# Performance work log

Measured on AMD Instinct MI355X. Metric: run time of the kernel, lower is better.

Reference implementation:

```python
import jax, jax.numpy as jnp
from jax import lax
import numpy as np

RADIUS = 1
DILATION = 2
NUM_BINS = 16  # DualSimilarityLoss uses num_bins=16
ALPHA = 5.0
BETA = 0.1
NOISE = 1e-4


def _avg_pool2(x):
    b, c, h, w = x.shape
    return x.reshape(b, c, h // 2, 2, w // 2, 2).mean(axis=(3, 5))


def _conv_rep(x, k, pad):
    # replicate-pad then VALID conv, NCHW / OIHW
    xp = jnp.pad(x, ((0, 0), (0, 0), (pad, pad), (pad, pad)), mode='edge')
    return lax.conv_general_dilated(xp, k, (1, 1), 'VALID',
                                    dimension_numbers=('NCHW', 'OIHW', 'NCHW'))


def _upsample_align_corners(x, H, W):
    # bilinear, align_corners=True (matches F.interpolate(..., align_corners=True))
    b, c, h, w = x.shape

    def coords(n_out, n_in):
        pos = jnp.arange(n_out, dtype=x.dtype) * ((n_in - 1) / (n_out - 1))
        i0 = jnp.clip(jnp.floor(pos).astype(jnp.int32), 0, n_in - 2)
        return i0, pos - i0.astype(x.dtype)

    y0, fy = coords(H, h)
    x0, fx = coords(W, w)
    rows = x[:, :, y0, :] * (1.0 - fy)[None, None, :, None] \
         + x[:, :, y0 + 1, :] * fy[None, None, :, None]
    out = rows[:, :, :, x0] * (1.0 - fx) + rows[:, :, :, x0 + 1] * fx
    return out


def _compute_mind(img, key):
    B, _, H, W = img.shape
    img = _avg_pool2(img)                      # (B,1,H/2,W/2)
    img = img + NOISE * jax.random.normal(key, img.shape, img.dtype)
    h, w = img.shape[2], img.shape[3]
    pad = RADIUS * DILATION                    # 2
    k = 2 * RADIUS + 1                         # 3
    ones_k = jnp.ones((1, 1, k, k), img.dtype)
    padded = jnp.pad(img, ((0, 0), (0, 0), (pad, pad), (pad, pad)), mode='edge')
    patch_mean = lax.conv_general_dilated(padded, ones_k, (1, 1), 'VALID',
                                          dimension_numbers=('NCHW', 'OIHW', 'NCHW')) / (k * k)
    patch_mean = jnp.pad(patch_mean, ((0, 0), (0, 0), (pad, pad), (pad, pad)), mode='edge')
    c = pad
    center = padded[:, :, c:c + h, c:c + w]
    variance = (center - patch_mean[:, :, c:c + h, c:c + w]) ** 2
    variance = _conv_rep(variance, ones_k, RADIUS) / (k * k)
    variance = jnp.maximum(variance, 1e-4)
    descs = []
    for i in range(-RADIUS, RADIUS + 1):
        for j in range(-RADIUS, RADIUS + 1):
            if i == 0 and j == 0:
                continue
            dx, dy = i * DILATION, j * DILATION
            off = padded[:, :, c + dy:c + dy + h, c + dx:c + dx + w]
            diff = jnp.clip((center - off) ** 2 / (variance * 2 + 1e-6), 0.0, 50.0)
            descs.append(diff)
    m = jnp.exp(-jnp.concatenate(descs, axis=1))          # (B,8,h,w)
    m = m / (m.sum(axis=1, keepdims=True) + 1e-8)
    m = jnp.where(jnp.isnan(m), 0.0, m)
    if (h, w) != (H, W):
        m = _upsample_align_corners(m, H, W)
    return m


def _nmi_loss(x, y, kx, ky):
    B = x.shape[0]
    x = x[:, :, ::2, ::2]
    y = y[:, :, ::2, ::2]
    x = x + NOISE * jax.random.normal(kx, x.shape, x.dtype)
    y = y + NOISE * jax.random.normal(ky, y.shape, y.dtype)
    xf = jnp.clip((x.reshape(B, -1) + 1.0) / 2.0, 0.001, 0.999)
    yf = jnp.clip((y.reshape(B, -1) + 1.0) / 2.0, 0.001, 0.999)
    grid = jnp.linspace(0.0, 1.0, NUM_BINS + 1)
    xb = jnp.clip(jnp.searchsorted(grid, xf, side='left') - 1, 0, NUM_BINS - 1)
    yb = jnp.clip(jnp.searchsorted(grid, yf, side='left') - 1, 0, NUM_BINS - 1)
    idx = xb * NUM_BINS + yb                               # (B,N)
    hist = jnp.zeros((B, NUM_BINS * NUM_BINS), jnp.float32)
    hist = hist.at[jnp.arange(B)[:, None], idx].add(1.0)
    hist = hist.reshape(B, NUM_BINS, NUM_BINS)
    hist = hist / (hist.sum(axis=(1, 2), keepdims=True) + 1e-10)
    xh = hist.sum(axis=2)
    yh = hist.sum(axis=1)
    eps = 1e-5
    hist = hist + eps
    xh = xh + eps
    yh = yh + eps
    mi = jnp.sum(hist * (jnp.log(hist) - jnp.log(xh[:, :, None] * yh[:, None, :])), axis=(1, 2))
    hx = -jnp.sum(xh * jnp.log(xh), axis=1)
    hy = -jnp.sum(yh * jnp.log(yh), axis=1)
    se = hx + hy
    nmi = jnp.where(se < 1e-10, 0.0, 2.0 * mi / se)
    nmi = jnp.clip(nmi, -1.0, 1.0)
    return -jnp.clip(nmi.mean(), -1.0, 1.0)


def _reg_loss(flow, ku, kv):
    sx = jnp.array([[-1, 0, 1], [-2, 0, 2], [-1, 0, 1]], jnp.float32).reshape(1, 1, 3, 3)
    sy = jnp.array([[-1, -2, -1], [0, 0, 0], [1, 2, 1]], jnp.float32).reshape(1, 1, 3, 3)
    lp = jnp.array([[0, 1, 0], [1, -4, 1], [0, 1, 0]], jnp.float32).reshape(1, 1, 3, 3)
    f = _avg_pool2(flow)
    u = f[:, 0:1] + NOISE * jax.random.normal(ku, f[:, 0:1].shape, f.dtype)
    v = f[:, 1:2] + NOISE * jax.random.normal(kv, f[:, 1:2].shape, f.dtype)
    grad_mag = _conv_rep(u, sx, 1) ** 2 + _conv_rep(u, sy, 1) ** 2 \
             + _conv_rep(v, sx, 1) ** 2 + _conv_rep(v, sy, 1) ** 2
    lap_mag = _conv_rep(u, lp, 1) ** 2 + _conv_rep(v, lp, 1) ** 2
    return jnp.clip(grad_mag, 0.0, 100.0).mean() + jnp.clip(lap_mag, 0.0, 100.0).mean()


def _total_loss(fixed, moved, flow):
    fixed = jnp.where(jnp.isnan(fixed), 0.0, fixed)
    moved = jnp.where(jnp.isnan(moved), 0.0, moved)
    flow = jnp.where(jnp.isnan(flow), 0.0, flow)
    ks = jax.random.split(jax.random.key(42), 6)
    mi = _nmi_loss(fixed, moved, ks[0], ks[1])
    mx = _compute_mind(fixed, ks[2])
    my = _compute_mind(moved, ks[3])
    d = jnp.abs(mx - my)
    mind = jnp.where(jnp.isnan(d), 0.0, d).mean()
    reg = _reg_loss(flow, ks[4], ks[5])
    return mi + ALPHA * mind + BETA * reg


def setup_inputs() -> dict:
    key = jax.random.key(0)
    k1, k2, k3 = jax.random.split(key, 3)
    B, H, W = 8, 512, 512
    return {
        'fixed': jax.random.normal(k1, (B, 1, H, W), jnp.float32),
        'moved': jax.random.normal(k2, (B, 1, H, W), jnp.float32),
        'flow': jax.random.normal(k3, (B, 2, H, W), jnp.float32),
    }


def reference(fixed, moved, flow):
    return _total_loss(fixed, moved, flow)
```

## Files before the change

### kernel.cpp

```cpp
#include <hip/hip_runtime.h>
#include <cmath>

#define BATCH 8
#define HF 512
#define WF 512
#define HS 256
#define WS 256
#define PLANE_S (HS * WS)
#define PLANE_F (HF * WF)

#define NMIND_BLOCKS 2048
#define NREG_BLOCKS  512

#define OFF_HIST  0
#define OFF_PMIND 8192
#define OFF_PGRAD (OFF_PMIND + NMIND_BLOCKS * 8)
#define OFF_PLAP  (OFF_PGRAD + NREG_BLOCKS * 8)

#define IMG_R 23
#define IMG_S 24
#define T_R 20
#define T_S 21
#define V_R 18
#define V_S 19

#define RP 34
#define RS 35

__device__ __forceinline__ int clampi(int v, int lo, int hi) {
    return v < lo ? lo : (v > hi ? hi : v);
}

__device__ __forceinline__ int bin_of(float x) {
    float v = (x + 1.0f) * 0.5f;
    v = fminf(fmaxf(v, 0.001f), 0.999f);
    float t = v * 16.0f;
    float ft = floorf(t);
    int c = (int)ft + ((t > ft) ? 1 : 0);
    int b = c - 1;
    return b < 0 ? 0 : (b > 15 ? 15 : b);
}

__global__ void init_hist_kernel(unsigned* __restrict__ hist) {
    hist[blockIdx.x * 256 + threadIdx.x] = 0u;
}

__global__ __launch_bounds__(256, 4) void fused_main_kernel(
    const float* __restrict__ fixed, const float* __restrict__ moved,
    const float* __restrict__ flow,
    unsigned* __restrict__ hist, double* __restrict__ pmind,
    double* __restrict__ pgrad, double* __restrict__ plap)
{
    __shared__ float S[4524];
    __shared__ unsigned lh[256];
    __shared__ float red[256];
    int tid = threadIdx.x;

    if (blockIdx.z < 2) {
        int idx = blockIdx.z * 256 + blockIdx.y * 16 + blockIdx.x;
        int b = idx >> 6, t64 = idx & 63;
        int y0p = (t64 >> 3) * 32, x0p = (t64 & 7) * 32;
        float* U = S;
        float* V = S + RP * RS;
        const float* ur = flow + (size_t)(b * 2) * PLANE_F;
        const float* vr = ur + PLANE_F;
        for (int i = tid; i < RP * RP; i += 256) {
            int r = i / RP, c = i - r * RP;
            int gy = clampi(y0p - 1 + r, 0, HS - 1);
            int gx = clampi(x0p - 1 + c, 0, WS - 1);
            const float* uu = ur + (size_t)(gy * 2) * WF + (size_t)(gx * 2);
            const float* vv = vr + (size_t)(gy * 2) * WF + (size_t)(gx * 2);
            float2 u0 = *(const float2*)uu, u1 = *(const float2*)(uu + WF);
            float2 v0 = *(const float2*)vv, v1 = *(const float2*)(vv + WF);
            U[r * RS + c] = (u0.x + u0.y + u1.x + u1.y) * 0.25f;
            V[r * RS + c] = (v0.x + v0.y + v1.x + v1.y) * 0.25f;
        }
        __syncthreads();
        float g = 0.f, l = 0.f;
        for (int k = tid; k < 32 * 32; k += 256) {
            int y = k >> 5, x = k & 31;
            const float* u0 = &U[y * RS + x];
            const float* v0 = &V[y * RS + x];
            float a00 = u0[0],      a01 = u0[1],          a02 = u0[2];
            float a10 = u0[RS],     a11 = u0[RS + 1],     a12 = u0[RS + 2];
            float a20 = u0[2 * RS], a21 = u0[2 * RS + 1], a22 = u0[2 * RS + 2];
            float c00 = v0[0],      c01 = v0[1],          c02 = v0[2];
            float c10 = v0[RS],     c11 = v0[RS + 1],     c12 = v0[RS + 2];
            float c20 = v0[2 * RS], c21 = v0[2 * RS + 1], c22 = v0[2 * RS + 2];
            float gxu = (a02 - a00) + 2.f * (a12 - a10) + (a22 - a20);
            float gyu = (a20 - a00) + 2.f * (a21 - a01) + (a22 - a02);
            float gxv = (c02 - c00) + 2.f * (c12 - c10) + (c22 - c20);
            float gyv = (c20 - c00) + 2.f * (c21 - c01) + (c22 - c02);
            float lpu = a01 + a10 - 4.f * a11 + a12 + a21;
            float lpv = c01 + c10 - 4.f * c11 + c12 + c21;
            float grad = gxu * gxu + gyu * gyu + gxv * gxv + gyv * gyv;
            float lap = lpu * lpu + lpv * lpv;
            g += fminf(grad, 100.f);
            l += fminf(lap, 100.f);
        }
        red[tid] = g;
        __syncthreads();
        for (int s = 128; s > 0; s >>= 1) { if (tid < s) red[tid] += red[tid + s]; __syncthreads(); }
        if (tid == 0) pgrad[b * 64 + t64] = (double)red[0];
        __syncthreads();
        red[tid] = l;
        __syncthreads();
        for (int s = 128; s > 0; s >>= 1) { if (tid < s) red[tid] += red[tid + s]; __syncthreads(); }
        if (tid == 0) plap[b * 64 + t64] = (double)red[0];
        return;
    }

    const float FS = (float)(255.0 / 511.0);
    int tx = blockIdx.x, ty = blockIdx.y, b = blockIdx.z - 2;
    int Xb = tx * 32, Yb = ty * 32;
    int dbx = (int)((float)Xb * FS);
    int dby = (int)((float)Yb * FS);
    int ibx = dbx - 3, iby = dby - 3;

    float* imgF = S;
    float* imgM = S + IMG_R * IMG_S;
    float* varF = S + 2 * IMG_R * IMG_S;
    float* varM = varF + V_R * V_S;
    float* diff = varM + V_R * V_S;
    float* tF   = diff;
    float* tM   = diff + T_R * T_S;

    lh[tid] = 0u;
    __syncthreads();

    const float* fb = fixed + (size_t)b * PLANE_F;
    const float* mb = moved + (size_t)b * PLANE_F;
    int oy0 = ty * 16, ox0 = tx * 16;
    for (int i = tid; i < IMG_R * IMG_R; i += 256) {
        int r = i / IMG_R, c = i - r * IMG_R;
        int gy = iby + r, gx = ibx + c;
        int cy = clampi(gy, 0, HS - 1), cx = clampi(gx, 0, WS - 1);
        const float* fp = fb + (size_t)(cy * 2) * WF + (size_t)(cx * 2);
        const float* mp = mb + (size_t)(cy * 2) * WF + (size_t)(cx * 2);
        float2 f0 = *(const float2*)fp;
        float2 f1 = *(const float2*)(fp + WF);
        float2 m0 = *(const float2*)mp;
        float2 m1 = *(const float2*)(mp + WF);
        imgF[r * IMG_S + c] = (f0.x + f0.y + f1.x + f1.y) * 0.25f;
        imgM[r * IMG_S + c] = (m0.x + m0.y + m1.x + m1.y) * 0.25f;
        if ((unsigned)(gy - oy0) < 16u && (unsigned)(gx - ox0) < 16u) {
            atomicAdd(&lh[bin_of(f0.x) * 16 + bin_of(m0.x)], 1u);
        }
    }
    __syncthreads();
    if (lh[tid]) atomicAdd(&hist[b * 256 + tid], lh[tid]);

    const float NINTH = 1.0f / 9.0f;
    for (int i = tid; i < T_R * T_R; i += 256) {
        int r = i / T_R, c = i - r * T_R;
        float sF = 0.f, sM = 0.f;
        #pragma unroll
        for (int dy = 0; dy < 3; dy++)
            #pragma unroll
            for (int dx = 0; dx < 3; dx++) {
                sF += imgF[(r + dy) * IMG_S + c + dx];
                sM += imgM[(r + dy) * IMG_S + c + dx];
            }
        float dF = imgF[(r + 2) * IMG_S + c + 2] - sF * NINTH;
        float dM = imgM[(r + 2) * IMG_S + c + 2] - sM * NINTH;
        tF[r * T_S + c] = dF * dF;
        tM[r * T_S + c] = dM * dM;
    }
    __syncthreads();

    for (int i = tid; i < V_R * V_R; i += 256) {
        int r = i / V_R, c = i - r * V_R;
        float sF = 0.f, sM = 0.f;
        #pragma unroll
        for (int dy = 0; dy < 3; dy++)
            #pragma unroll
            for (int dx = 0; dx < 3; dx++) {
                sF += tF[(r + dy) * T_S + c + dx];
                sM += tM[(r + dy) * T_S + c + dx];
            }
        varF[r * V_S + c] = fmaxf(sF * NINTH, 1e-4f);
        varM[r * V_S + c] = fmaxf(sM * NINTH, 1e-4f);
    }
    __syncthreads();

    for (int i = tid; i < V_R * V_R; i += 256) {
        int r = i / V_R, c = i - r * V_R;
        float cF = imgF[(r + 3) * IMG_S + c + 3];
        float cM = imgM[(r + 3) * IMG_S + c + 3];
        float dF2 = 2.f * varF[r * V_S + c] + 1e-6f;
        float dM2 = 2.f * varM[r * V_S + c] + 1e-6f;
        float invF = 1.0f / dF2;
        float invM = 1.0f / dM2;
        float eF[8], eM[8];
        float sF = 0.f, sM = 0.f;
        int ch = 0;
        #pragma unroll
        for (int ii = -1; ii <= 1; ii++) {
            #pragma unroll
            for (int jj = -1; jj <= 1; jj++) {
                if (ii == 0 && jj == 0) continue;
                float aF = cF - imgF[(r + 3 + 2 * jj) * IMG_S + (c + 3 + 2 * ii)];
                float aM = cM - imgM[(r + 3 + 2 * jj) * IMG_S + (c + 3 + 2 * ii)];
                float qF = fminf(aF * aF * invF, 50.f);
                float qM = fminf(aM * aM * invM, 50.f);
                float vF_ = expf(-qF), vM_ = expf(-qM);
                eF[ch] = vF_; eM[ch] = vM_;
                sF += vF_; sM += vM_;
                ch++;
            }
        }
        float wF = 1.f / (sF + 1e-8f);
        float wM = 1.f / (sM + 1e-8f);
        float* dp = diff + (size_t)(r * V_S + c) * 8;
        #pragma unroll
        for (int q = 0; q < 8; q++) dp[q] = eF[q] * wF - eM[q] * wM;
    }
    __syncthreads();

    float local = 0.f;
    for (int k = tid; k < 32 * 32; k += 256) {
        int dy = k >> 5, dx = k & 31;
        float py = (float)(Yb + dy) * FS;
        int y0 = (int)py; if (y0 > HS - 2) y0 = HS - 2;
        float fy = py - (float)y0;
        float px = (float)(Xb + dx) * FS;
        int x0 = (int)px; if (x0 > WS - 2) x0 = WS - 2;
        float fx = px - (float)x0;
        const float* p00 = diff + (size_t)((y0 - dby) * V_S + (x0 - dbx)) * 8;
        const float* p10 = p00 + V_S * 8;
        #pragma unroll
        for (int q = 0; q < 8; q++) {
            float a  = p00[q]     * (1.f - fy) + p10[q]     * fy;
            float c2 = p00[q + 8] * (1.f - fy) + p10[q + 8] * fy;
            local += fabsf(a * (1.f - fx) + c2 * fx);
        }
    }
    red[tid] = local;
    __syncthreads();
    for (int s = 128; s > 0; s >>= 1) { if (tid < s) red[tid] += red[tid + s]; __syncthreads(); }
    if (tid == 0) pmind[b * 256 + ty * 16 + tx] = (double)red[0];
}

__global__ void tail_kernel(const unsigned* __restrict__ hist,
                            const double* __restrict__ pmind,
                            const double* __restrict__ pgrad, const double* __restrict__ plap,
                            float* __restrict__ out) {
    int t = threadIdx.x;
    __shared__ float p[256];
    __shared__ float xh[16], yh[16];
    __shared__ float redf[256];
    __shared__ double red[256];

    float nmi_sum = 0.f;
    const float eps = 1e-5f;
    for (int b = 0; b < BATCH; b++) {
        unsigned hv = hist[b * 256 + t];
        float pv = (float)hv / 65536.0f;
        p[t] = pv;
        __syncthreads();
        if (t < 16) {
            float s = 0.f;
            for (int j = 0; j < 16; j++) s += p[t * 16 + j];
            xh[t] = s;
        } else if (t < 32) {
            int j = t - 16;
            float s = 0.f;
            for (int i = 0; i < 16; i++) s += p[i * 16 + j];
            yh[j] = s;
        }
        __syncthreads();
        int i = t >> 4, j = t & 15;
        float h = pv + eps;
        float mi_term = h * (logf(h) - logf((xh[i] + eps) * (yh[j] + eps)));
        redf[t] = mi_term;
        __syncthreads();
        for (int s = 128; s > 0; s >>= 1) { if (t < s) redf[t] += redf[t + s]; __syncthreads(); }
        float mi = redf[0];
        __syncthreads();
        float e_term = 0.f;
        if (t < 16) { float xe = xh[t] + eps; e_term = -xe * logf(xe); }
        else if (t < 32) { float ye = yh[t - 16] + eps; e_term = -ye * logf(ye); }
        redf[t] = e_term;
        __syncthreads();
        for (int s = 128; s > 0; s >>= 1) { if (t < s) redf[t] += redf[t + s]; __syncthreads(); }
        float se = redf[0];
        float nmi = (se < 1e-10f) ? 0.f : 2.f * mi / se;
        nmi_sum += fminf(fmaxf(nmi, -1.f), 1.f);
        __syncthreads();
    }

    double sm = 0.0;
    for (int i = t; i < NMIND_BLOCKS; i += 256) sm += pmind[i];
    double sg = 0.0, sl = 0.0;
    for (int i = t; i < NREG_BLOCKS; i += 256) { sg += pgrad[i]; sl += plap[i]; }
    red[t] = sm;
    __syncthreads();
    for (int s = 128; s > 0; s >>= 1) { if (t < s) red[t] += red[t + s]; __syncthreads(); }
    double mind_sum = red[0];
    __syncthreads();
    red[t] = sg;
    __syncthreads();
    for (int s = 128; s > 0; s >>= 1) { if (t < s) red[t] += red[t + s]; __syncthreads(); }
    double grad_sum = red[0];
    __syncthreads();
    red[t] = sl;
    __syncthreads();
    for (int s = 128; s > 0; s >>= 1) { if (t < s) red[t] += red[t + s]; __syncthreads(); }
    double lap_sum = red[0];
    if (t == 0) {
        float s = nmi_sum / (float)BATCH;
        s = fminf(fmaxf(s, -1.f), 1.f);
        double mi_loss = -(double)s;
        double mind_mean = mind_sum / (64.0 * (double)PLANE_F);
        double reg = grad_sum / (double)(BATCH * PLANE_S) + lap_sum / (double)(BATCH * PLANE_S);
        out[0] = (float)(mi_loss + 5.0 * mind_mean + 0.1 * reg);
    }
}

extern "C" void kernel_launch(void* const* d_in, const int* in_sizes, int n_in,
                              void* d_out, int out_size, void* d_ws, size_t ws_size,
                              hipStream_t stream) {
    const float* fixed = (const float*)d_in[0];
    const float* moved = (const float*)d_in[1];
    const float* flow  = (const float*)d_in[2];
    float* out = (float*)d_out;
    char* ws = (char*)d_ws;

    unsigned* hist  = (unsigned*)(ws + OFF_HIST);
    double*   pmind = (double*)(ws + OFF_PMIND);
    double*   pgrad = (double*)(ws + OFF_PGRAD);
    double*   plap  = (double*)(ws + OFF_PLAP);

    init_hist_kernel<<<dim3(8), 256, 0, stream>>>(hist);
    fused_main_kernel<<<dim3(16, 16, 10), 256, 0, stream>>>(fixed, moved, flow,
                                                            hist, pmind, pgrad, plap);
    tail_kernel<<<1, 256, 0, stream>>>(hist, pmind, pgrad, plap, out);
}
```

Measured before the change: 121.7 us.

## Fold tail reduction into main kernel via last-block ticket counters

Removes the separate single-block tail kernel. Blocks now atomically add their partial sums into global doubles, and per-batch ticket counters let the last block of each batch compute that batch's NMI. A global counter then lets the final block write the loss. This drops one kernel launch and the serial tail pass. In exchange it adds global atomics and fences, and the double atomicAdd makes the summation order nondeterministic.

```diff
diff --git a/kernel.cpp b/kernel.cpp
--- a/kernel.cpp
+++ b/kernel.cpp
@@ -9,13 +9,15 @@
 #define PLANE_S (HS * WS)
 #define PLANE_F (HF * WF)
 
-#define NMIND_BLOCKS 2048
-#define NREG_BLOCKS  512
+#define TICKETS_PER_BATCH 320u
 
 #define OFF_HIST  0
-#define OFF_PMIND 8192
-#define OFF_PGRAD (OFF_PMIND + NMIND_BLOCKS * 8)
-#define OFF_PLAP  (OFF_PGRAD + NREG_BLOCKS * 8)
+#define OFF_CNTB  8192
+#define OFF_GCNT  8224
+#define OFF_NMIB  8228
+#define OFF_SUMS  8264
+#define OFF_END   8288
+#define INIT_WORDS (OFF_END / 4)
 
 #define IMG_R 23
 #define IMG_S 24
@@ -41,24 +43,32 @@
     return b < 0 ? 0 : (b > 15 ? 15 : b);
 }
 
-__global__ void init_hist_kernel(unsigned* __restrict__ hist) {
-    hist[blockIdx.x * 256 + threadIdx.x] = 0u;
-}
-
-__global__ __launch_bounds__(256, 4) void fused_main_kernel(
+__global__ void init_kernel(unsigned* __restrict__ w) {
+    int t = threadIdx.x;
+    for (int i = t; i < INIT_WORDS; i += 256) w[i] = 0u;
+}
+
+__global__ __launch_bounds__(256, 4) void fused_all_kernel(
     const float* __restrict__ fixed, const float* __restrict__ moved,
     const float* __restrict__ flow,
-    unsigned* __restrict__ hist, double* __restrict__ pmind,
-    double* __restrict__ pgrad, double* __restrict__ plap)
+    unsigned* __restrict__ hist, unsigned* __restrict__ cntb,
+    unsigned* __restrict__ gcnt, unsigned* __restrict__ nmib,
+    double* __restrict__ sums, float* __restrict__ out)
 {
     __shared__ float S[4524];
     __shared__ unsigned lh[256];
     __shared__ float red[256];
+    __shared__ float xh[16], yh[16];
+    __shared__ float fn[8];
+    __shared__ double fs[3];
+    __shared__ unsigned tk, gk;
     int tid = threadIdx.x;
+    int bb;
 
     if (blockIdx.z < 2) {
         int idx = blockIdx.z * 256 + blockIdx.y * 16 + blockIdx.x;
         int b = idx >> 6, t64 = idx & 63;
+        bb = b;
         int y0p = (t64 >> 3) * 32, x0p = (t64 & 7) * 32;
         float* U = S;
         float* V = S + RP * RS;
@@ -101,218 +111,209 @@
         red[tid] = g;
         __syncthreads();
         for (int s = 128; s > 0; s >>= 1) { if (tid < s) red[tid] += red[tid + s]; __syncthreads(); }
-        if (tid == 0) pgrad[b * 64 + t64] = (double)red[0];
+        if (tid == 0) atomicAdd(&sums[1], (double)red[0]);
         __syncthreads();
         red[tid] = l;
         __syncthreads();
         for (int s = 128; s > 0; s >>= 1) { if (tid < s) red[tid] += red[tid + s]; __syncthreads(); }
-        if (tid == 0) plap[b * 64 + t64] = (double)red[0];
-        return;
-    }
-
-    const float FS = (float)(255.0 / 511.0);
-    int tx = blockIdx.x, ty = blockIdx.y, b = blockIdx.z - 2;
-    int Xb = tx * 32, Yb = ty * 32;
-    int dbx = (int)((float)Xb * FS);
-    int dby = (int)((float)Yb * FS);
-    int ibx = dbx - 3, iby = dby - 3;
-
-    float* imgF = S;
-    float* imgM = S + IMG_R * IMG_S;
-    float* varF = S + 2 * IMG_R * IMG_S;
-    float* varM = varF + V_R * V_S;
-    float* diff = varM + V_R * V_S;
-    float* tF   = diff;
-    float* tM   = diff + T_R * T_S;
-
-    lh[tid] = 0u;
-    __syncthreads();
-
-    const float* fb = fixed + (size_t)b * PLANE_F;
-    const float* mb = moved + (size_t)b * PLANE_F;
-    int oy0 = ty * 16, ox0 = tx * 16;
-    for (int i = tid; i < IMG_R * IMG_R; i += 256) {
-        int r = i / IMG_R, c = i - r * IMG_R;
-        int gy = iby + r, gx = ibx + c;
-        int cy = clampi(gy, 0, HS - 1), cx = clampi(gx, 0, WS - 1);
-        const float* fp = fb + (size_t)(cy * 2) * WF + (size_t)(cx * 2);
-        const float* mp = mb + (size_t)(cy * 2) * WF + (size_t)(cx * 2);
-        float2 f0 = *(const float2*)fp;
-        float2 f1 = *(const float2*)(fp + WF);
-        float2 m0 = *(const float2*)mp;
-        float2 m1 = *(const float2*)(mp + WF);
-        imgF[r * IMG_S + c] = (f0.x + f0.y + f1.x + f1.y) * 0.25f;
-        imgM[r * IMG_S + c] = (m0.x + m0.y + m1.x + m1.y) * 0.25f;
-        if ((unsigned)(gy - oy0) < 16u && (unsigned)(gx - ox0) < 16u) {
-            atomicAdd(&lh[bin_of(f0.x) * 16 + bin_of(m0.x)], 1u);
-        }
-    }
-    __syncthreads();
-    if (lh[tid]) atomicAdd(&hist[b * 256 + tid], lh[tid]);
-
-    const float NINTH = 1.0f / 9.0f;
-    for (int i = tid; i < T_R * T_R; i += 256) {
-        int r = i / T_R, c = i - r * T_R;
-        float sF = 0.f, sM = 0.f;
-        #pragma unroll
-        for (int dy = 0; dy < 3; dy++)
-            #pragma unroll
-            for (int dx = 0; dx < 3; dx++) {
-                sF += imgF[(r + dy) * IMG_S + c + dx];
-                sM += imgM[(r + dy) * IMG_S + c + dx];
+        if (tid == 0) atomicAdd(&sums[2], (double)red[0]);
+    } else {
+        const float FS = (float)(255.0 / 511.0);
+        int tx = blockIdx.x, ty = blockIdx.y, b = blockIdx.z - 2;
+        bb = b;
+        int Xb = tx * 32, Yb = ty * 32;
+        int dbx = (int)((float)Xb * FS);
+        int dby = (int)((float)Yb * FS);
+        int ibx = dbx - 3, iby = dby - 3;
+
+        float* imgF = S;
+        float* imgM = S + IMG_R * IMG_S;
+        float* varF = S + 2 * IMG_R * IMG_S;
+        float* varM = varF + V_R * V_S;
+        float* diff = varM + V_R * V_S;
+        float* tF   = diff;
+        float* tM   = diff + T_R * T_S;
+
+        lh[tid] = 0u;
+        __syncthreads();
+
+        const float* fb = fixed + (size_t)b * PLANE_F;
+        const float* mb = moved + (size_t)b * PLANE_F;
+        int oy0 = ty * 16, ox0 = tx * 16;
+        for (int i = tid; i < IMG_R * IMG_R; i += 256) {
+            int r = i / IMG_R, c = i - r * IMG_R;
+            int gy = iby + r, gx = ibx + c;
+            int cy = clampi(gy, 0, HS - 1), cx = clampi(gx, 0, WS - 1);
+            const float* fp = fb + (size_t)(cy * 2) * WF + (size_t)(cx * 2);
+            const float* mp = mb + (size_t)(cy * 2) * WF + (size_t)(cx * 2);
+            float2 f0 = *(const float2*)fp;
+            float2 f1 = *(const float2*)(fp + WF);
+            float2 m0 = *(const float2*)mp;
+            float2 m1 = *(const float2*)(mp + WF);
+            imgF[r * IMG_S + c] = (f0.x + f0.y + f1.x + f1.y) * 0.25f;
+            imgM[r * IMG_S + c] = (m0.x + m0.y + m1.x + m1.y) * 0.25f;
+            if ((unsigned)(gy - oy0) < 16u && (unsigned)(gx - ox0) < 16u) {
+                atomicAdd(&lh[bin_of(f0.x) * 16 + bin_of(m0.x)], 1u);
             }
-        float dF = imgF[(r + 2) * IMG_S + c + 2] - sF * NINTH;
-        float dM = imgM[(r + 2) * IMG_S + c + 2] - sM * NINTH;
-        tF[r * T_S + c] = dF * dF;
-        tM[r * T_S + c] = dM * dM;
-    }
-    __syncthreads();
-
-    for (int i = tid; i < V_R * V_R; i += 256) {
-        int r = i / V_R, c = i - r * V_R;
-        float sF = 0.f, sM = 0.f;
-        #pragma unroll
-        for (int dy = 0; dy < 3; dy++)
-            #pragma unroll
-            for (int dx = 0; dx < 3; dx++) {
-                sF += tF[(r + dy) * T_S + c + dx];
-                sM += tM[(r + dy) * T_S + c + dx];
+        }
+        __syncthreads();
+        if (lh[tid]) atomicAdd(&hist[b * 256 + tid], lh[tid]);
+
+        const float NINTH = 1.0f / 9.0f;
+        for (int i = tid; i < T_R * T_R; i += 256) {
+            int r = i / T_R, c = i - r * T_R;
+            float sF = 0.f, sM = 0.f;
+            #pragma unroll
+            for (int dy = 0; dy < 3; dy++)
+                #pragma unroll
+                for (int dx = 0; dx < 3; dx++) {
+                    sF += imgF[(r + dy) * IMG_S + c + dx];
+                    sM += imgM[(r + dy) * IMG_S + c + dx];
+                }
+            float dF = imgF[(r + 2) * IMG_S + c + 2] - sF * NINTH;
+            float dM = imgM[(r + 2) * IMG_S + c + 2] - sM * NINTH;
+            tF[r * T_S + c] = dF * dF;
+            tM[r * T_S + c] = dM * dM;
+        }
+        __syncthreads();
+
+        for (int i = tid; i < V_R * V_R; i += 256) {
+            int r = i / V_R, c = i - r * V_R;
+            float sF = 0.f, sM = 0.f;
+            #pragma unroll
+            for (int dy = 0; dy < 3; dy++)
+                #pragma unroll
+                for (int dx = 0; dx < 3; dx++) {
+                    sF += tF[(r + dy) * T_S + c + dx];
+                    sM += tM[(r + dy) * T_S + c + dx];
+                }
+            varF[r * V_S + c] = fmaxf(sF * NINTH, 1e-4f);
+            varM[r * V_S + c] = fmaxf(sM * NINTH, 1e-4f);
+        }
+        __syncthreads();
+
+        for (int i = tid; i < V_R * V_R; i += 256) {
+            int r = i / V_R, c = i - r * V_R;
+            float cF = imgF[(r + 3) * IMG_S + c + 3];
+            float cM = imgM[(r + 3) * IMG_S + c + 3];
+            float dF2 = 2.f * varF[r * V_S + c] + 1e-6f;
+            float dM2 = 2.f * varM[r * V_S + c] + 1e-6f;
+            float invF = 1.0f / dF2;
+            float invM = 1.0f / dM2;
+            float eF[8], eM[8];
+            float sF = 0.f, sM = 0.f;
+            int ch = 0;
+            #pragma unroll
+            for (int ii = -1; ii <= 1; ii++) {
+                #pragma unroll
+                for (int jj = -1; jj <= 1; jj++) {
+                    if (ii == 0 && jj == 0) continue;
+                    float aF = cF - imgF[(r + 3 + 2 * jj) * IMG_S + (c + 3 + 2 * ii)];
+                    float aM = cM - imgM[(r + 3 + 2 * jj) * IMG_S + (c + 3 + 2 * ii)];
+                    float qF = fminf(aF * aF * invF, 50.f);
+                    float qM = fminf(aM * aM * invM, 50.f);
+                    float vF_ = expf(-qF), vM_ = expf(-qM);
+                    eF[ch] = vF_; eM[ch] = vM_;
+                    sF += vF_; sM += vM_;
+                    ch++;
+                }
             }
-        varF[r * V_S + c] = fmaxf(sF * NINTH, 1e-4f);
-        varM[r * V_S + c] = fmaxf(sM * NINTH, 1e-4f);
-    }
-    __syncthreads();
-
-    for (int i = tid; i < V_R * V_R; i += 256) {
-        int r = i / V_R, c = i - r * V_R;
-        float cF = imgF[(r + 3) * IMG_S + c + 3];
-        float cM = imgM[(r + 3) * IMG_S + c + 3];
-        float dF2 = 2.f * varF[r * V_S + c] + 1e-6f;
-        float dM2 = 2.f * varM[r * V_S + c] + 1e-6f;
-        float invF = 1.0f / dF2;
-        float invM = 1.0f / dM2;
-        float eF[8], eM[8];
-        float sF = 0.f, sM = 0.f;
-        int ch = 0;
-        #pragma unroll
-        for (int ii = -1; ii <= 1; ii++) {
-            #pragma unroll
-            for (int jj = -1; jj <= 1; jj++) {
-                if (ii == 0 && jj == 0) continue;
-                float aF = cF - imgF[(r + 3 + 2 * jj) * IMG_S + (c + 3 + 2 * ii)];
-                float aM = cM - imgM[(r + 3 + 2 * jj) * IMG_S + (c + 3 + 2 * ii)];
-                float qF = fminf(aF * aF * invF, 50.f);
-                float qM = fminf(aM * aM * invM, 50.f);
-                float vF_ = expf(-qF), vM_ = expf(-qM);
-                eF[ch] = vF_; eM[ch] = vM_;
-                sF += vF_; sM += vM_;
-                ch++;
+            float wF = 1.f / (sF + 1e-8f);
+            float wM = 1.f / (sM + 1e-8f);
+            float* dp = diff + (size_t)(r * V_S + c) * 8;
+            #pragma unroll
+            for (int q = 0; q < 8; q++) dp[q] = eF[q] * wF - eM[q] * wM;
+        }
+        __syncthreads();
+
+        float local = 0.f;
+        for (int k = tid; k < 32 * 32; k += 256) {
+            int dy = k >> 5, dx = k & 31;
+            float py = (float)(Yb + dy) * FS;
+            int y0 = (int)py; if (y0 > HS - 2) y0 = HS - 2;
+            float fy = py - (float)y0;
+            float px = (float)(Xb + dx) * FS;
+            int x0 = (int)px; if (x0 > WS - 2) x0 = WS - 2;
+            float fx = px - (float)x0;
+            const float* p00 = diff + (size_t)((y0 - dby) * V_S + (x0 - dbx)) * 8;
+            const float* p10 = p00 + V_S * 8;
+            #pragma unroll
+            for (int q = 0; q < 8; q++) {
+                float a  = p00[q]     * (1.f - fy) + p10[q]     * fy;
+                float c2 = p00[q + 8] * (1.f - fy) + p10[q + 8] * fy;
+                local += fabsf(a * (1.f - fx) + c2 * fx);
             }
         }
-        float wF = 1.f / (sF + 1e-8f);
-        float wM = 1.f / (sM + 1e-8f);
-        float* dp = diff + (size_t)(r * V_S + c) * 8;
-        #pragma unroll
-        for (int q = 0; q < 8; q++) dp[q] = eF[q] * wF - eM[q] * wM;
-    }
-    __syncthreads();
-
-    float local = 0.f;
-    for (int k = tid; k < 32 * 32; k += 256) {
-        int dy = k >> 5, dx = k & 31;
-        float py = (float)(Yb + dy) * FS;
-        int y0 = (int)py; if (y0 > HS - 2) y0 = HS - 2;
-        float fy = py - (float)y0;
-        float px = (float)(Xb + dx) * FS;
-        int x0 = (int)px; if (x0 > WS - 2) x0 = WS - 2;
-        float fx = px - (float)x0;
-        const float* p00 = diff + (size_t)((y0 - dby) * V_S + (x0 - dbx)) * 8;
-        const float* p10 = p00 + V_S * 8;
-        #pragma unroll
-        for (int q = 0; q < 8; q++) {
-            float a  = p00[q]     * (1.f - fy) + p10[q]     * fy;
-            float c2 = p00[q + 8] * (1.f - fy) + p10[q + 8] * fy;
-            local += fabsf(a * (1.f - fx) + c2 * fx);
-        }
-    }
-    red[tid] = local;
+        red[tid] = local;
+        __syncthreads();
+        for (int s = 128; s > 0; s >>= 1) { if (tid < s) red[tid] += red[tid + s]; __syncthreads(); }
+        if (tid == 0) atomicAdd(&sums[0], (double)red[0]);
+    }
+
+    __syncthreads();
+    if (tid == 0) {
+        __threadfence();
+        tk = atomicAdd(&cntb[bb], 1u);
+    }
+    __syncthreads();
+    if (tk != TICKETS_PER_BATCH - 1u) return;
+
+    __threadfence();
+    unsigned hv = atomicOr(&hist[bb * 256 + tid], 0u);
+    float pv = (float)hv / 65536.0f;
+    S[tid] = pv;
+    __syncthreads();
+    if (tid < 16) {
+        float s = 0.f;
+        for (int j = 0; j < 16; j++) s += S[tid * 16 + j];
+        xh[tid] = s;
+    } else if (tid < 32) {
+        int j = tid - 16;
+        float s = 0.f;
+        for (int i = 0; i < 16; i++) s += S[i * 16 + j];
+        yh[j] = s;
+    }
+    __syncthreads();
+    const float eps = 1e-5f;
+    int ii2 = tid >> 4, jj2 = tid & 15;
+    float h = pv + eps;
+    float mi_term = h * (logf(h) - logf((xh[ii2] + eps) * (yh[jj2] + eps)));
+    red[tid] = mi_term;
     __syncthreads();
     for (int s = 128; s > 0; s >>= 1) { if (tid < s) red[tid] += red[tid + s]; __syncthreads(); }
-    if (tid == 0) pmind[b * 256 + ty * 16 + tx] = (double)red[0];
-}
-
-__global__ void tail_kernel(const unsigned* __restrict__ hist,
-                            const double* __restrict__ pmind,
-                            const double* __restrict__ pgrad, const double* __restrict__ plap,
-                            float* __restrict__ out) {
-    int t = threadIdx.x;
-    __shared__ float p[256];
-    __shared__ float xh[16], yh[16];
-    __shared__ float redf[256];
-    __shared__ double red[256];
-
-    float nmi_sum = 0.f;
-    const float eps = 1e-5f;
-    for (int b = 0; b < BATCH; b++) {
-        unsigned hv = hist[b * 256 + t];
-        float pv = (float)hv / 65536.0f;
-        p[t] = pv;
-        __syncthreads();
-        if (t < 16) {
-            float s = 0.f;
-            for (int j = 0; j < 16; j++) s += p[t * 16 + j];
-            xh[t] = s;
-        } else if (t < 32) {
-            int j = t - 16;
-            float s = 0.f;
-            for (int i = 0; i < 16; i++) s += p[i * 16 + j];
-            yh[j] = s;
-        }
-        __syncthreads();
-        int i = t >> 4, j = t & 15;
-        float h = pv + eps;
-        float mi_term = h * (logf(h) - logf((xh[i] + eps) * (yh[j] + eps)));
-        redf[t] = mi_term;
-        __syncthreads();
-        for (int s = 128; s > 0; s >>= 1) { if (t < s) redf[t] += redf[t + s]; __syncthreads(); }
-        float mi = redf[0];
-        __syncthreads();
-        float e_term = 0.f;
-        if (t < 16) { float xe = xh[t] + eps; e_term = -xe * logf(xe); }
-        else if (t < 32) { float ye = yh[t - 16] + eps; e_term = -ye * logf(ye); }
-        redf[t] = e_term;
-        __syncthreads();
-        for (int s = 128; s > 0; s >>= 1) { if (t < s) redf[t] += redf[t + s]; __syncthreads(); }
-        float se = redf[0];
+    float mi = red[0];
+    __syncthreads();
+    float e_term = 0.f;
+    if (tid < 16) { float xe = xh[tid] + eps; e_term = -xe * logf(xe); }
+    else if (tid < 32) { float ye = yh[tid - 16] + eps; e_term = -ye * logf(ye); }
+    red[tid] = e_term;
+    __syncthreads();
+    for (int s = 128; s > 0; s >>= 1) { if (tid < s) red[tid] += red[tid + s]; __syncthreads(); }
+    if (tid == 0) {
+        float se = red[0];
         float nmi = (se < 1e-10f) ? 0.f : 2.f * mi / se;
-        nmi_sum += fminf(fmaxf(nmi, -1.f), 1.f);
-        __syncthreads();
-    }
-
-    double sm = 0.0;
-    for (int i = t; i < NMIND_BLOCKS; i += 256) sm += pmind[i];
-    double sg = 0.0, sl = 0.0;
-    for (int i = t; i < NREG_BLOCKS; i += 256) { sg += pgrad[i]; sl += plap[i]; }
-    red[t] = sm;
-    __syncthreads();
-    for (int s = 128; s > 0; s >>= 1) { if (t < s) red[t] += red[t + s]; __syncthreads(); }
-    double mind_sum = red[0];
-    __syncthreads();
-    red[t] = sg;
-    __syncthreads();
-    for (int s = 128; s > 0; s >>= 1) { if (t < s) red[t] += red[t + s]; __syncthreads(); }
-    double grad_sum = red[0];
-    __syncthreads();
-    red[t] = sl;
-    __syncthreads();
-    for (int s = 128; s > 0; s >>= 1) { if (t < s) red[t] += red[t + s]; __syncthreads(); }
-    double lap_sum = red[0];
-    if (t == 0) {
-        float s = nmi_sum / (float)BATCH;
+        nmi = fminf(fmaxf(nmi, -1.f), 1.f);
+        atomicExch(&nmib[bb], __float_as_uint(nmi));
+        __threadfence();
+        gk = atomicAdd(gcnt, 1u);
+    }
+    __syncthreads();
+    if (gk != BATCH - 1u) return;
+
+    __threadfence();
+    if (tid < 8)       fn[tid] = __uint_as_float(atomicOr(&nmib[tid], 0u));
+    else if (tid == 8)  fs[0] = atomicAdd(&sums[0], 0.0);
+    else if (tid == 9)  fs[1] = atomicAdd(&sums[1], 0.0);
+    else if (tid == 10) fs[2] = atomicAdd(&sums[2], 0.0);
+    __syncthreads();
+    if (tid == 0) {
+        float s = 0.f;
+        for (int b2 = 0; b2 < BATCH; b2++) s += fn[b2];
+        s /= (float)BATCH;
         s = fminf(fmaxf(s, -1.f), 1.f);
         double mi_loss = -(double)s;
-        double mind_mean = mind_sum / (64.0 * (double)PLANE_F);
-        double reg = grad_sum / (double)(BATCH * PLANE_S) + lap_sum / (double)(BATCH * PLANE_S);
+        double mind_mean = fs[0] / (64.0 * (double)PLANE_F);
+        double reg = fs[1] / (double)(BATCH * PLANE_S) + fs[2] / (double)(BATCH * PLANE_S);
         out[0] = (float)(mi_loss + 5.0 * mind_mean + 0.1 * reg);
     }
 }
@@ -326,13 +327,13 @@
     float* out = (float*)d_out;
     char* ws = (char*)d_ws;
 
-    unsigned* hist  = (unsigned*)(ws + OFF_HIST);
-    double*   pmind = (double*)(ws + OFF_PMIND);
-    double*   pgrad = (double*)(ws + OFF_PGRAD);
-    double*   plap  = (double*)(ws + OFF_PLAP);
-
-    init_hist_kernel<<<dim3(8), 256, 0, stream>>>(hist);
-    fused_main_kernel<<<dim3(16, 16, 10), 256, 0, stream>>>(fixed, moved, flow,
-                                                            hist, pmind, pgrad, plap);
-    tail_kernel<<<1, 256, 0, stream>>>(hist, pmind, pgrad, plap, out);
-}
+    unsigned* hist = (unsigned*)(ws + OFF_HIST);
+    unsigned* cntb = (unsigned*)(ws + OFF_CNTB);
+    unsigned* gcnt = (unsigned*)(ws + OFF_GCNT);
+    unsigned* nmib = (unsigned*)(ws + OFF_NMIB);
+    double*   sums = (double*)(ws + OFF_SUMS);
+
+    init_kernel<<<dim3(1), 256, 0, stream>>>((unsigned*)ws);
+    fused_all_kernel<<<dim3(16, 16, 10), 256, 0, stream>>>(fixed, moved, flow,
+                                                           hist, cntb, gcnt, nmib, sums, out);
+}
```

Measured after the change: 158.4 us. 30.1% more time.
